# Optimization experiments

Measured on AMD Instinct MI355X. Metric: run time of the kernel, lower is better.

## Reference

```python
import jax, jax.numpy as jnp
import numpy as np

QUERY_DIM = 1024
KV_DIM = 768
NUM_HEADS = 16
HEAD_DIM = QUERY_DIM // NUM_HEADS


def setup_inputs() -> dict:
    key = jax.random.key(0)
    ks = jax.random.split(key, 11)
    B, Sq, Skv = 4, 2048, 2048
    s_q = 1.0 / np.sqrt(QUERY_DIM)
    s_kv = 1.0 / np.sqrt(KV_DIM)
    return {
        "query": jax.random.normal(ks[0], (B, Sq, QUERY_DIM), jnp.float32),
        "key": jax.random.normal(ks[1], (B, Skv, KV_DIM), jnp.float32),
        "value": jax.random.normal(ks[2], (B, Skv, KV_DIM), jnp.float32),
        "Wq": jax.random.uniform(ks[3], (QUERY_DIM, QUERY_DIM), jnp.float32, -s_q, s_q),
        "bq": jax.random.uniform(ks[4], (QUERY_DIM,), jnp.float32, -s_q, s_q),
        "Wk": jax.random.uniform(ks[5], (KV_DIM, QUERY_DIM), jnp.float32, -s_kv, s_kv),
        "bk": jax.random.uniform(ks[6], (QUERY_DIM,), jnp.float32, -s_kv, s_kv),
        "Wv": jax.random.uniform(ks[7], (KV_DIM, QUERY_DIM), jnp.float32, -s_kv, s_kv),
        "bv": jax.random.uniform(ks[8], (QUERY_DIM,), jnp.float32, -s_kv, s_kv),
        "Wo": jax.random.uniform(ks[9], (QUERY_DIM, QUERY_DIM), jnp.float32, -s_q, s_q),
        "bo": jax.random.uniform(ks[10], (QUERY_DIM,), jnp.float32, -s_q, s_q),
    }


def reference(query, key, value, Wq, bq, Wk, bk, Wv, bv, Wo, bo):
    B, Sq, _ = query.shape
    Skv = key.shape[1]
    H, D = NUM_HEADS, HEAD_DIM
    # linear projections, then split heads: [B, H, S, D]
    q = (query @ Wq + bq).reshape(B, Sq, H, D).transpose(0, 2, 1, 3)
    k = (key @ Wk + bk).reshape(B, Skv, H, D).transpose(0, 2, 1, 3)
    v = (value @ Wv + bv).reshape(B, Skv, H, D).transpose(0, 2, 1, 3)
    scores = jnp.einsum("bhqd,bhkd->bhqk", q, k) / np.sqrt(D).astype(jnp.float32)
    probs = jax.nn.softmax(scores, axis=-1)
    ctx = jnp.einsum("bhqk,bhkd->bhqd", probs, v)
    ctx = ctx.transpose(0, 2, 1, 3).reshape(B, Sq, H * D)
    return ctx @ Wo + bo
```

## Files before the change

### kernel.cpp

```cpp
#include <hip/hip_runtime.h>

typedef unsigned short u16;
typedef unsigned int u32;
typedef unsigned long long u64;
typedef __attribute__((ext_vector_type(8))) short bf16x8;
typedef __attribute__((ext_vector_type(4))) float f32x4;

__device__ __forceinline__ u16 f2bf(float f) {
  union { float f; u32 u; } v; v.f = f;
  u32 r = v.u + 0x7fffu + ((v.u >> 16) & 1u);
  return (u16)(r >> 16);
}
__device__ __forceinline__ u32 pack2bf(float a, float b) {
  union { float f; u32 u; } x, y; x.f = a; y.f = b;
  return ((y.u + 0x8000u) & 0xffff0000u) | ((x.u + 0x8000u) >> 16);
}

__device__ __forceinline__ void gll16(const u16* g, u16* l) {
  __builtin_amdgcn_global_load_lds((__attribute__((address_space(1))) void*)(void*)g,
                                   (__attribute__((address_space(3))) void*)(void*)l,
                                   16, 0, 0);
}

#define SCALE_C 0.18033688011112042f

__global__ void conv_bf16(const float* __restrict__ in, u16* __restrict__ out, int n) {
  int i = (blockIdx.x * 256 + threadIdx.x) * 4;
  if (i < n) {
    float4 v = *(const float4*)(in + i);
    ushort4 o;
    o.x = f2bf(v.x); o.y = f2bf(v.y); o.z = f2bf(v.z); o.w = f2bf(v.w);
    *(ushort4*)(out + i) = o;
  }
}

__global__ void transpose_bf16(const float* __restrict__ W, u16* __restrict__ T,
                               int K, int N) {
  __shared__ u16 tile[64 * 72];
  const int k0 = blockIdx.x * 64, n0 = blockIdx.y * 64;
  const int t = threadIdx.x, c = t & 63, rb = t >> 6;
#pragma unroll
  for (int rr = 0; rr < 64; rr += 4) {
    int r = rr + rb;
    tile[r * 72 + c] = f2bf(W[(size_t)(k0 + r) * N + n0 + c]);
  }
  __syncthreads();
#pragma unroll
  for (int rr = 0; rr < 64; rr += 4) {
    int n = rr + rb;
    T[(size_t)(n0 + n) * K + k0 + c] = tile[c * 72 + n];
  }
}

__global__ __launch_bounds__(256, 3) void gemm_qkv(
    const u16* __restrict__ Aq, const u16* __restrict__ Ak, const u16* __restrict__ Av,
    const u16* __restrict__ Bwq, const u16* __restrict__ Bwk, const u16* __restrict__ Bwv,
    const float* __restrict__ bq, const float* __restrict__ bk, const float* __restrict__ bv,
    u16* __restrict__ oq, u16* __restrict__ ok, u16* __restrict__ ov) {
  const int z = blockIdx.z;
  const u16* A = (z == 0) ? Aq : (z == 1) ? Ak : Av;
  const u16* Bt = (z == 0) ? Bwq : (z == 1) ? Bwk : Bwv;
  const float* bias = (z == 0) ? bq : (z == 1) ? bk : bv;
  u16* outb = (z == 0) ? oq : (z == 1) ? ok : ov;
  const int K = (z == 0) ? 1024 : 768;
  const float scale = (z == 0) ? SCALE_C : 1.0f;
  __shared__ __align__(16) u16 smem[18432];
  u16* lA = smem;
  u16* lB = smem + 128 * 64;
  const int tid = threadIdx.x;
  const int bm = blockIdx.x * 128;
  const int bn = blockIdx.y * 128;
  const int wid = tid >> 6, lane = tid & 63;
  const int wm = (wid >> 1) * 64, wn = (wid & 1) * 64;
  const int lrow = lane & 15, quad = lane >> 4;
  const int wrow = lane >> 3, wchk = lane & 7;
  const int sw = lrow & 7;
  f32x4 acc[4][4] = {};
  for (int k0 = 0; k0 < K; k0 += 64) {
    const u16* gA = A + (size_t)(bm + wid * 32) * K + k0;
    const u16* gB = Bt + (size_t)(bn + wid * 32) * K + k0;
#pragma unroll
    for (int c = 0; c < 4; c++) {
      gll16(gA + (size_t)(c * 8 + wrow) * K + (wchk ^ wrow) * 8, &lA[(wid * 32 + c * 8) * 64]);
      gll16(gB + (size_t)(c * 8 + wrow) * K + (wchk ^ wrow) * 8, &lB[(wid * 32 + c * 8) * 64]);
    }
    __syncthreads();
#pragma unroll
    for (int ks = 0; ks < 2; ks++) {
      bf16x8 af[4], bfr[4];
#pragma unroll
      for (int i = 0; i < 4; i++)
        af[i] = *(const bf16x8*)&lA[(wm + i * 16 + lrow) * 64 + ((ks * 4 + quad) ^ sw) * 8];
#pragma unroll
      for (int j = 0; j < 4; j++)
        bfr[j] = *(const bf16x8*)&lB[(wn + j * 16 + lrow) * 64 + ((ks * 4 + quad) ^ sw) * 8];
#pragma unroll
      for (int i = 0; i < 4; i++)
#pragma unroll
        for (int j = 0; j < 4; j++)
          acc[i][j] = __builtin_amdgcn_mfma_f32_16x16x32_bf16(af[i], bfr[j], acc[i][j], 0, 0, 0);
    }
    __syncthreads();
  }
  if (z == 2) {
    u16* tile = smem + wid * (64 * 72);
#pragma unroll
    for (int i = 0; i < 4; i++)
#pragma unroll
      for (int j = 0; j < 4; j++)
#pragma unroll
        for (int r = 0; r < 4; r++) {
          int s_l = i * 16 + quad * 4 + r;
          int d_l = j * 16 + lrow;
          tile[d_l * 72 + s_l] = f2bf(acc[i][j][r] + bias[bn + wn + d_l]);
        }
    __syncthreads();
#pragma unroll
    for (int dd = 0; dd < 8; dd++) {
      int d_l = dd * 8 + (lane >> 3);
      int s_l = (lane & 7) * 8;
      bf16x8 vv = *(const bf16x8*)&tile[d_l * 72 + s_l];
      int row = bm + wm + s_l;
      int col = bn + wn + d_l;
      int b = row >> 11, s = row & 2047;
      int h = col >> 6, d = col & 63;
      *(bf16x8*)&outb[((size_t)(b * 16 + h) * 64 + d) * 2048 + s] = vv;
    }
    return;
  }
#pragma unroll
  for (int i = 0; i < 4; i++)
#pragma unroll
    for (int j = 0; j < 4; j++)
#pragma unroll
      for (int r = 0; r < 4; r++) {
        int row = bm + wm + i * 16 + quad * 4 + r;
        int col = bn + wn + j * 16 + lrow;
        float v = (acc[i][j][r] + bias[col]) * scale;
        int b = row >> 11, s = row & 2047;
        int h = col >> 6, d = col & 63;
        outb[((size_t)(b * 16 + h) * 2048 + s) * 64 + d] = f2bf(v);
      }
}

__global__ __launch_bounds__(256, 3) void gemm_out(
    const u16* __restrict__ A, const u16* __restrict__ Bt,
    const float* __restrict__ bias, float* __restrict__ outf) {
  __shared__ __align__(16) u16 smem[16384];
  u16* lA = smem;
  u16* lB = smem + 128 * 64;
  const int tid = threadIdx.x;
  const int bm = blockIdx.x * 128;
  const int bn = blockIdx.y * 128;
  const int wid = tid >> 6, lane = tid & 63;
  const int wm = (wid >> 1) * 64, wn = (wid & 1) * 64;
  const int lrow = lane & 15, quad = lane >> 4;
  const int wrow = lane >> 3, wchk = lane & 7;
  const int sw = lrow & 7;
  f32x4 acc[4][4] = {};
  for (int k0 = 0; k0 < 1024; k0 += 64) {
    const u16* gA = A + (size_t)(bm + wid * 32) * 1024 + k0;
    const u16* gB = Bt + (size_t)(bn + wid * 32) * 1024 + k0;
#pragma unroll
    for (int c = 0; c < 4; c++) {
      gll16(gA + (size_t)(c * 8 + wrow) * 1024 + (wchk ^ wrow) * 8, &lA[(wid * 32 + c * 8) * 64]);
      gll16(gB + (size_t)(c * 8 + wrow) * 1024 + (wchk ^ wrow) * 8, &lB[(wid * 32 + c * 8) * 64]);
    }
    __syncthreads();
#pragma unroll
    for (int ks = 0; ks < 2; ks++) {
      bf16x8 af[4], bfr[4];
#pragma unroll
      for (int i = 0; i < 4; i++)
        af[i] = *(const bf16x8*)&lA[(wm + i * 16 + lrow) * 64 + ((ks * 4 + quad) ^ sw) * 8];
#pragma unroll
      for (int j = 0; j < 4; j++)
        bfr[j] = *(const bf16x8*)&lB[(wn + j * 16 + lrow) * 64 + ((ks * 4 + quad) ^ sw) * 8];
#pragma unroll
      for (int i = 0; i < 4; i++)
#pragma unroll
        for (int j = 0; j < 4; j++)
          acc[i][j] = __builtin_amdgcn_mfma_f32_16x16x32_bf16(af[i], bfr[j], acc[i][j], 0, 0, 0);
    }
    __syncthreads();
  }
#pragma unroll
  for (int i = 0; i < 4; i++)
#pragma unroll
    for (int j = 0; j < 4; j++)
#pragma unroll
      for (int r = 0; r < 4; r++) {
        int row = bm + wm + i * 16 + quad * 4 + r;
        int col = bn + wn + j * 16 + lrow;
        outf[(size_t)row * 1024 + col] = acc[i][j][r] + bias[col];
      }
}

__global__ __launch_bounds__(256, 2) void flash_attn(
    const u16* __restrict__ Q, const u16* __restrict__ Kt,
    const u16* __restrict__ Vt, u16* __restrict__ ctx) {
  __shared__ __align__(16) u16 smem[10752];
  const int tid = threadIdx.x, wid = tid >> 6, lane = tid & 63;
  u16* lP = smem + wid * 2560;
  const int bh = blockIdx.x;
  const int q0 = blockIdx.y * 64;
  const int lrow = lane & 15, quad = lane >> 4;
  const size_t base = (size_t)bh * 2048 * 64;
  bf16x8 qf[4][2];
#pragma unroll
  for (int qt = 0; qt < 4; qt++)
#pragma unroll
    for (int ks = 0; ks < 2; ks++)
      qf[qt][ks] = *(const bf16x8*)(Q + base + (size_t)(q0 + qt * 16 + lrow) * 64 + ks * 32 + quad * 8);
  f32x4 of[4][4] = {};
  float lsumq[4] = {0.f, 0.f, 0.f, 0.f};
  for (int kv0 = 0; kv0 < 2048; kv0 += 128) {
    const int kvw = kv0 + wid * 32;
    bf16x8 kf[2][2], vf[4];
#pragma unroll
    for (int nt = 0; nt < 2; nt++)
#pragma unroll
      for (int ks = 0; ks < 2; ks++)
        kf[nt][ks] = *(const bf16x8*)(Kt + base + (size_t)(kvw + nt * 16 + lrow) * 64 + ks * 32 + quad * 8);
#pragma unroll
    for (int dt = 0; dt < 4; dt++)
      vf[dt] = *(const bf16x8*)(Vt + base + (size_t)(dt * 16 + lrow) * 2048 + kvw + quad * 8);
    f32x4 sfT[2][4];
#pragma unroll
    for (int nt = 0; nt < 2; nt++)
#pragma unroll
      for (int qt = 0; qt < 4; qt++) {
        f32x4 s = {};
        s = __builtin_amdgcn_mfma_f32_16x16x32_bf16(kf[nt][0], qf[qt][0], s, 0, 0, 0);
        s = __builtin_amdgcn_mfma_f32_16x16x32_bf16(kf[nt][1], qf[qt][1], s, 0, 0, 0);
        sfT[nt][qt] = s;
      }
#pragma unroll
    for (int nt = 0; nt < 2; nt++)
#pragma unroll
      for (int qt = 0; qt < 4; qt++) {
        float p0 = __builtin_amdgcn_exp2f(sfT[nt][qt][0]);
        float p1 = __builtin_amdgcn_exp2f(sfT[nt][qt][1]);
        float p2 = __builtin_amdgcn_exp2f(sfT[nt][qt][2]);
        float p3 = __builtin_amdgcn_exp2f(sfT[nt][qt][3]);
        lsumq[qt] += (p0 + p1) + (p2 + p3);
        u64 pk = ((u64)pack2bf(p2, p3) << 32) | pack2bf(p0, p1);
        *(u64*)&lP[(qt * 16 + lrow) * 40 + nt * 16 + quad * 4] = pk;
      }
    __asm__ volatile("s_waitcnt lgkmcnt(0)" ::: "memory");
#pragma unroll
    for (int qt = 0; qt < 4; qt++) {
      bf16x8 pf = *(const bf16x8*)&lP[(qt * 16 + lrow) * 40 + quad * 8];
#pragma unroll
      for (int dt = 0; dt < 4; dt++)
        of[qt][dt] = __builtin_amdgcn_mfma_f32_16x16x32_bf16(pf, vf[dt], of[qt][dt], 0, 0, 0);
    }
  }
  float lsw[4];
#pragma unroll
  for (int qt = 0; qt < 4; qt++) {
    float v = lsumq[qt];
    v += __shfl_xor(v, 16, 64);
    v += __shfl_xor(v, 32, 64);
    lsw[qt] = v;
  }
  __syncthreads();
  float* lsums = (float*)(smem + 10240);
  if (quad == 0) {
#pragma unroll
    for (int qt = 0; qt < 4; qt++) lsums[wid * 64 + qt * 16 + lrow] = lsw[qt];
  }
  float* rbuf = (float*)smem;
  for (int w = 0; w < 4; w++) {
    if (wid == w) {
#pragma unroll
      for (int qt = 0; qt < 4; qt++)
#pragma unroll
        for (int dt = 0; dt < 4; dt++)
#pragma unroll
          for (int r = 0; r < 4; r++) {
            int q = qt * 16 + quad * 4 + r;
            int d = dt * 16 + lrow;
            if (w == 0) rbuf[q * 66 + d] = of[qt][dt][r];
            else        rbuf[q * 66 + d] += of[qt][dt][r];
          }
    }
    __syncthreads();
  }
  const int b = bh >> 4, h = bh & 15;
#pragma unroll
  for (int it = 0; it < 2; it++) {
    int q = wid * 16 + it * 8 + (lane >> 3);
    int d0 = (lane & 7) * 8;
    float inv = 1.f / (lsums[q] + lsums[64 + q] + lsums[128 + q] + lsums[192 + q]);
    u16 o[8];
#pragma unroll
    for (int j = 0; j < 8; j++) o[j] = f2bf(rbuf[q * 66 + d0 + j] * inv);
    *(bf16x8*)&ctx[((size_t)b * 2048 + q0 + q) * 1024 + h * 64 + d0] = *(bf16x8*)o;
  }
}

extern "C" void kernel_launch(void* const* d_in, const int* in_sizes, int n_in,
                              void* d_out, int out_size, void* d_ws, size_t ws_size,
                              hipStream_t stream) {
  const float* query = (const float*)d_in[0];
  const float* key   = (const float*)d_in[1];
  const float* value = (const float*)d_in[2];
  const float* Wq = (const float*)d_in[3];
  const float* bq = (const float*)d_in[4];
  const float* Wk = (const float*)d_in[5];
  const float* bk = (const float*)d_in[6];
  const float* Wv = (const float*)d_in[7];
  const float* bv = (const float*)d_in[8];
  const float* Wo = (const float*)d_in[9];
  const float* bo = (const float*)d_in[10];
  float* out = (float*)d_out;
  char* ws = (char*)d_ws;

  const size_t SZ_QKV = (size_t)8192 * 1024 * 2;
  const size_t SZ_KIN = (size_t)8192 * 768 * 2;
  u16* q_ws  = (u16*)(ws);
  u16* k_ws  = (u16*)(ws + SZ_QKV);
  u16* vt_ws = (u16*)(ws + 2 * SZ_QKV);
  u16* qin   = (u16*)(ws + 3 * SZ_QKV);
  u16* kin   = (u16*)(ws + 4 * SZ_QKV);
  u16* vin   = (u16*)(ws + 4 * SZ_QKV + SZ_KIN);
  u16* ctx   = qin;
  u16* wq_t  = (u16*)(ws + 4 * SZ_QKV + 2 * SZ_KIN);
  u16* wk_t  = wq_t + 1024 * 1024;
  u16* wv_t  = wk_t + 1024 * 768;
  u16* wo_t  = wv_t + 1024 * 768;

  conv_bf16<<<8192, 256, 0, stream>>>(query, qin, 8388608);
  conv_bf16<<<6144, 256, 0, stream>>>(key, kin, 6291456);
  conv_bf16<<<6144, 256, 0, stream>>>(value, vin, 6291456);
  transpose_bf16<<<dim3(16, 16), 256, 0, stream>>>(Wq, wq_t, 1024, 1024);
  transpose_bf16<<<dim3(12, 16), 256, 0, stream>>>(Wk, wk_t, 768, 1024);
  transpose_bf16<<<dim3(12, 16), 256, 0, stream>>>(Wv, wv_t, 768, 1024);
  transpose_bf16<<<dim3(16, 16), 256, 0, stream>>>(Wo, wo_t, 1024, 1024);

  gemm_qkv<<<dim3(64, 8, 3), 256, 0, stream>>>(qin, kin, vin, wq_t, wk_t, wv_t,
                                               bq, bk, bv, q_ws, k_ws, vt_ws);

  flash_attn<<<dim3(64, 32), 256, 0, stream>>>(q_ws, k_ws, vt_ws, ctx);

  gemm_out<<<dim3(64, 8), 256, 0, stream>>>(ctx, wo_t, bo, out);
}
```

Before: 386.7 us.

## Double-buffer K tiles in LDS, stage QKV epilogue, merge prep kernels

The flash attention kernel now streams K tiles into a double-buffered, XOR-swizzled LDS area with asynchronous global-to-LDS loads, prefetching the next tile while computing the current one. Occupancy is raised to 3 blocks per SM despite the larger shared allocation. The Q/K projection epilogue now goes through an LDS tile so global writes are 16-byte vectors instead of scalar bf16 stores. The three conversion launches and four weight transposes are each merged into a single launch to cut launch overhead. The larger LDS footprint and the higher launch bound may limit residency or cause register spills.

```diff
diff --git a/kernel.cpp b/kernel.cpp
--- a/kernel.cpp
+++ b/kernel.cpp
@@ -24,25 +24,38 @@
 
 #define SCALE_C 0.18033688011112042f
 
-__global__ void conv_bf16(const float* __restrict__ in, u16* __restrict__ out, int n) {
-  int i = (blockIdx.x * 256 + threadIdx.x) * 4;
-  if (i < n) {
-    float4 v = *(const float4*)(in + i);
-    ushort4 o;
-    o.x = f2bf(v.x); o.y = f2bf(v.y); o.z = f2bf(v.z); o.w = f2bf(v.w);
-    *(ushort4*)(out + i) = o;
-  }
-}
-
-__global__ void transpose_bf16(const float* __restrict__ W, u16* __restrict__ T,
-                               int K, int N) {
+__global__ void conv_bf16_all(const float* __restrict__ q, const float* __restrict__ k,
+                              const float* __restrict__ v, u16* __restrict__ oq,
+                              u16* __restrict__ ok, u16* __restrict__ ov) {
+  int blk = blockIdx.x;
+  const float* in; u16* out; int i;
+  if (blk < 8192)       { in = q; out = oq; i = blk * 256 + threadIdx.x; }
+  else if (blk < 14336) { in = k; out = ok; i = (blk - 8192) * 256 + threadIdx.x; }
+  else                  { in = v; out = ov; i = (blk - 14336) * 256 + threadIdx.x; }
+  i *= 4;
+  float4 vv = *(const float4*)(in + i);
+  ushort4 o;
+  o.x = f2bf(vv.x); o.y = f2bf(vv.y); o.z = f2bf(vv.z); o.w = f2bf(vv.w);
+  *(ushort4*)(out + i) = o;
+}
+
+__global__ void transpose_all(const float* __restrict__ Wq, const float* __restrict__ Wk,
+                              const float* __restrict__ Wv, const float* __restrict__ Wo,
+                              u16* __restrict__ tq, u16* __restrict__ tk,
+                              u16* __restrict__ tv, u16* __restrict__ to_) {
+  const int z = blockIdx.z;
+  const float* W = (z == 0) ? Wq : (z == 1) ? Wk : (z == 2) ? Wv : Wo;
+  u16* T = (z == 0) ? tq : (z == 1) ? tk : (z == 2) ? tv : to_;
+  const int K = (z == 0 || z == 3) ? 1024 : 768;
+  const int k0 = blockIdx.x * 64;
+  if (k0 >= K) return;
   __shared__ u16 tile[64 * 72];
-  const int k0 = blockIdx.x * 64, n0 = blockIdx.y * 64;
+  const int n0 = blockIdx.y * 64;
   const int t = threadIdx.x, c = t & 63, rb = t >> 6;
 #pragma unroll
   for (int rr = 0; rr < 64; rr += 4) {
     int r = rr + rb;
-    tile[r * 72 + c] = f2bf(W[(size_t)(k0 + r) * N + n0 + c]);
+    tile[r * 72 + c] = f2bf(W[(size_t)(k0 + r) * 1024 + n0 + c]);
   }
   __syncthreads();
 #pragma unroll
@@ -102,8 +115,8 @@
     }
     __syncthreads();
   }
+  u16* tile = smem + wid * (64 * 72);
   if (z == 2) {
-    u16* tile = smem + wid * (64 * 72);
 #pragma unroll
     for (int i = 0; i < 4; i++)
 #pragma unroll
@@ -134,13 +147,22 @@
     for (int j = 0; j < 4; j++)
 #pragma unroll
       for (int r = 0; r < 4; r++) {
-        int row = bm + wm + i * 16 + quad * 4 + r;
-        int col = bn + wn + j * 16 + lrow;
-        float v = (acc[i][j][r] + bias[col]) * scale;
-        int b = row >> 11, s = row & 2047;
-        int h = col >> 6, d = col & 63;
-        outb[((size_t)(b * 16 + h) * 2048 + s) * 64 + d] = f2bf(v);
+        int s_l = i * 16 + quad * 4 + r;
+        int d_l = j * 16 + lrow;
+        tile[s_l * 72 + d_l] = f2bf((acc[i][j][r] + bias[bn + wn + d_l]) * scale);
       }
+  __syncthreads();
+#pragma unroll
+  for (int it = 0; it < 8; it++) {
+    int s_l = it * 8 + (lane >> 3);
+    int d0 = (lane & 7) * 8;
+    bf16x8 vv = *(const bf16x8*)&tile[s_l * 72 + d0];
+    int row = bm + wm + s_l;
+    int col = bn + wn + d0;
+    int b = row >> 11, s = row & 2047;
+    int h = col >> 6, d = col & 63;
+    *(bf16x8*)&outb[((size_t)(b * 16 + h) * 2048 + s) * 64 + d] = vv;
+  }
 }
 
 __global__ __launch_bounds__(256, 3) void gemm_out(
@@ -196,16 +218,17 @@
       }
 }
 
-__global__ __launch_bounds__(256, 2) void flash_attn(
+__global__ __launch_bounds__(256, 3) void flash_attn(
     const u16* __restrict__ Q, const u16* __restrict__ Kt,
     const u16* __restrict__ Vt, u16* __restrict__ ctx) {
-  __shared__ __align__(16) u16 smem[10752];
+  __shared__ __align__(16) u16 smem[26624];
   const int tid = threadIdx.x, wid = tid >> 6, lane = tid & 63;
-  u16* lP = smem + wid * 2560;
+  u16* lP = smem + 16384 + wid * 2560;
   const int bh = blockIdx.x;
   const int q0 = blockIdx.y * 64;
   const int lrow = lane & 15, quad = lane >> 4;
   const size_t base = (size_t)bh * 2048 * 64;
+  const int wrow8 = lane >> 3, wchk8 = lane & 7;
   bf16x8 qf[4][2];
 #pragma unroll
   for (int qt = 0; qt < 4; qt++)
@@ -214,27 +237,44 @@
       qf[qt][ks] = *(const bf16x8*)(Q + base + (size_t)(q0 + qt * 16 + lrow) * 64 + ks * 32 + quad * 8);
   f32x4 of[4][4] = {};
   float lsumq[4] = {0.f, 0.f, 0.f, 0.f};
-  for (int kv0 = 0; kv0 < 2048; kv0 += 128) {
-    const int kvw = kv0 + wid * 32;
-    bf16x8 kf[2][2], vf[4];
-#pragma unroll
-    for (int nt = 0; nt < 2; nt++)
-#pragma unroll
-      for (int ks = 0; ks < 2; ks++)
-        kf[nt][ks] = *(const bf16x8*)(Kt + base + (size_t)(kvw + nt * 16 + lrow) * 64 + ks * 32 + quad * 8);
+  {
+    const u16* gK = Kt + base + (size_t)(wid * 32) * 64;
+    u16* dst = smem + wid * 2048;
+#pragma unroll
+    for (int c = 0; c < 4; c++)
+      gll16(gK + (size_t)(c * 8 + wrow8) * 64 + (wchk8 ^ wrow8) * 8, dst + c * 8 * 64);
+  }
+  for (int it = 0; it < 16; ++it) {
+    const int kvw = it * 128 + wid * 32;
+    const u16* lKw = smem + (it & 1) * 8192 + wid * 2048;
+    bf16x8 vf[4];
 #pragma unroll
     for (int dt = 0; dt < 4; dt++)
       vf[dt] = *(const bf16x8*)(Vt + base + (size_t)(dt * 16 + lrow) * 2048 + kvw + quad * 8);
+    __asm__ volatile("" ::: "memory");
+    if (it < 15) {
+      const u16* gK = Kt + base + (size_t)(kvw + 128) * 64;
+      u16* dst = smem + ((it + 1) & 1) * 8192 + wid * 2048;
+#pragma unroll
+      for (int c = 0; c < 4; c++)
+        gll16(gK + (size_t)(c * 8 + wrow8) * 64 + (wchk8 ^ wrow8) * 8, dst + c * 8 * 64);
+      __asm__ volatile("s_waitcnt vmcnt(8)" ::: "memory");
+    } else {
+      __asm__ volatile("s_waitcnt vmcnt(4)" ::: "memory");
+    }
     f32x4 sfT[2][4];
 #pragma unroll
-    for (int nt = 0; nt < 2; nt++)
+    for (int nt = 0; nt < 2; nt++) {
+      bf16x8 kf0 = *(const bf16x8*)&lKw[(nt * 16 + lrow) * 64 + (quad ^ (lrow & 7)) * 8];
+      bf16x8 kf1 = *(const bf16x8*)&lKw[(nt * 16 + lrow) * 64 + ((4 + quad) ^ (lrow & 7)) * 8];
 #pragma unroll
       for (int qt = 0; qt < 4; qt++) {
         f32x4 s = {};
-        s = __builtin_amdgcn_mfma_f32_16x16x32_bf16(kf[nt][0], qf[qt][0], s, 0, 0, 0);
-        s = __builtin_amdgcn_mfma_f32_16x16x32_bf16(kf[nt][1], qf[qt][1], s, 0, 0, 0);
+        s = __builtin_amdgcn_mfma_f32_16x16x32_bf16(kf0, qf[qt][0], s, 0, 0, 0);
+        s = __builtin_amdgcn_mfma_f32_16x16x32_bf16(kf1, qf[qt][1], s, 0, 0, 0);
         sfT[nt][qt] = s;
       }
+    }
 #pragma unroll
     for (int nt = 0; nt < 2; nt++)
 #pragma unroll
@@ -265,7 +305,7 @@
     lsw[qt] = v;
   }
   __syncthreads();
-  float* lsums = (float*)(smem + 10240);
+  float* lsums = (float*)(smem + 16384);
   if (quad == 0) {
 #pragma unroll
     for (int qt = 0; qt < 4; qt++) lsums[wid * 64 + qt * 16 + lrow] = lsw[qt];
@@ -331,18 +371,11 @@
   u16* wv_t  = wk_t + 1024 * 768;
   u16* wo_t  = wv_t + 1024 * 768;
 
-  conv_bf16<<<8192, 256, 0, stream>>>(query, qin, 8388608);
-  conv_bf16<<<6144, 256, 0, stream>>>(key, kin, 6291456);
-  conv_bf16<<<6144, 256, 0, stream>>>(value, vin, 6291456);
-  transpose_bf16<<<dim3(16, 16), 256, 0, stream>>>(Wq, wq_t, 1024, 1024);
-  transpose_bf16<<<dim3(12, 16), 256, 0, stream>>>(Wk, wk_t, 768, 1024);
-  transpose_bf16<<<dim3(12, 16), 256, 0, stream>>>(Wv, wv_t, 768, 1024);
-  transpose_bf16<<<dim3(16, 16), 256, 0, stream>>>(Wo, wo_t, 1024, 1024);
-
+  conv_bf16_all<<<20480, 256, 0, stream>>>(query, key, value, qin, kin, vin);
+  transpose_all<<<dim3(16, 16, 4), 256, 0, stream>>>(Wq, Wk, Wv, Wo,
+                                                     wq_t, wk_t, wv_t, wo_t);
   gemm_qkv<<<dim3(64, 8, 3), 256, 0, stream>>>(qin, kin, vin, wq_t, wk_t, wv_t,
                                                bq, bk, bv, q_ws, k_ws, vt_ws);
-
   flash_attn<<<dim3(64, 32), 256, 0, stream>>>(q_ws, k_ws, vt_ws, ctx);
-
   gemm_out<<<dim3(64, 8), 256, 0, stream>>>(ctx, wo_t, bo, out);
 }
```

New measurement: 340.1 us. 1.14x faster.
